# Optimization experiments

Measured on AMD Instinct MI355X. Metric: run time of the kernel, lower is better.

Reference implementation:

```python
import jax, jax.numpy as jnp
import numpy as np

N_CLASSES = 14
# n_classes==14 branch of the original: classes 0..6 -> 1 target maximum, 7..13 -> 2
NUM_TARGET = jnp.array([1] * 7 + [2] * 7, dtype=jnp.int32)
K_MAX = 2
MARGIN = 1.0  # margin=1, p=1 in the original loss_maxima calls


def _neighbor_max8(x):
    """Max over the 8-adjacent neighbors of each pixel (implicit 8-adjacency graph)."""
    H, W = x.shape
    pad = jnp.pad(x, 1, constant_values=-np.inf)
    shifts = [pad[di:di + H, dj:dj + W]
              for di in (0, 1, 2) for dj in (0, 1, 2) if not (di == 1 and dj == 1)]
    return jnp.max(jnp.stack(shifts, 0), axis=0)


def _channel_loss(x, k_target):
    """Surrogate of higra loss_maxima(graph, x, 'dynamics', 'volume', k, margin=1, p=1):
    strict 8-adjacency local maxima are ranked by importance (value above global min,
    a vectorizable proxy for dynamics/volume extinction); the top-k_target maxima pay a
    hinge max(0, margin - imp), all other maxima pay their importance (spurious peaks)."""
    imp = x - jnp.min(x)                      # persistence proxy, >= 0
    is_max = x > _neighbor_max8(x)            # strict local maxima on 8-adjacency
    total = jnp.sum(jnp.where(is_max, imp, 0.0))
    flat = jnp.where(is_max, imp, -np.inf).reshape(-1)
    topv, _ = jax.lax.top_k(flat, K_MAX)      # K_MAX=2 covers both branches
    valid = jnp.isfinite(topv) & (jnp.arange(K_MAX) < k_target)
    target_sum = jnp.sum(jnp.where(valid, topv, 0.0))
    spurious = total - target_sum             # penalize non-target maxima (volume proxy)
    hinge = jnp.sum(jnp.where(valid, jnp.maximum(MARGIN - topv, 0.0), 0.0))
    return spurious + hinge


def setup_inputs() -> dict:
    key = jax.random.key(0)
    k1, k2 = jax.random.split(key)
    inputs = jax.random.normal(k1, (1, N_CLASSES, 2048, 2048), dtype=jnp.float32)
    target = jax.random.randint(k2, (1, 2048, 2048), 0, N_CLASSES, dtype=jnp.int64)
    return {"inputs": inputs, "target": target}


def reference(inputs, target):
    # softmax=True path (logit inputs, as used in training)
    probs = jax.nn.softmax(inputs, axis=1)            # [1, C, H, W]
    onehot = jax.nn.one_hot(target, N_CLASSES, axis=1).astype(jnp.float32)
    assert probs.shape == onehot.shape                # mirrors original assert; onehot unused in loss
    chans = probs[0]                                  # only batch element 0, as in original
    losses = jax.vmap(_channel_loss)(chans, NUM_TARGET)
    return jnp.sum(losses) / N_CLASSES
```

## Files before the change

### kernel.cpp

```cpp
#include <hip/hip_runtime.h>

#define HH 2048
#define WW 2048
#define CC 14
#define TILE 30
#define NT 69
#define NB (NT*NT)
#define PB 4768

#define PINF __int_as_float(0x7f800000)
#define NINF __int_as_float(0xff800000)

template<int CTRL>
__device__ __forceinline__ float dppf(float x) {
  return __int_as_float(__builtin_amdgcn_update_dpp(0, __float_as_int(x), CTRL, 0xF, 0xF, true));
}
template<int CTRL>
__device__ __forceinline__ int dppi(int x) {
  return __builtin_amdgcn_update_dpp(0, x, CTRL, 0xF, 0xF, true);
}

struct Red { float mn, sm, t0, t1; int ct; };

template<int CTRL>
__device__ __forceinline__ void red_step(Red& r) {
  float omn = dppf<CTRL>(r.mn);
  float osm = dppf<CTRL>(r.sm);
  float o0  = dppf<CTRL>(r.t0);
  float o1  = dppf<CTRL>(r.t1);
  int   oc  = dppi<CTRL>(r.ct);
  r.mn = fminf(r.mn, omn);
  r.sm += osm;
  r.ct += oc;
  float n1 = fmaxf(fminf(r.t0, o0), fmaxf(r.t1, o1));
  r.t0 = fmaxf(r.t0, o0);
  r.t1 = n1;
}

__device__ __forceinline__ void wave_reduce(Red& r) {
  red_step<0xB1>(r);
  red_step<0x4E>(r);
  red_step<0x141>(r);
  red_step<0x140>(r);
  red_step<0x142>(r);
  red_step<0x143>(r);
}

__device__ __forceinline__ void merge2(float& a0, float& a1, float b0, float b1) {
  float n1 = fmaxf(fminf(a0, b0), fmaxf(a1, b1));
  a0 = fmaxf(a0, b0);
  a1 = n1;
}

__global__ __launch_bounds__(256, 2)
void k_main(const float* __restrict__ X, char* __restrict__ ws, int mode) {
  const int tid = threadIdx.x;
  const int bx = blockIdx.x, by = blockIdx.y;
  const int blk = by * NT + bx;
  const int rr = tid >> 3, c8 = tid & 7, c0 = c8 << 2;
  const int gr = by * TILE - 1 + rr;
  const int gc0 = bx * TILE - 1 + c0;
  const int lane = tid & 63, wv = tid >> 6;

  __shared__ float4 hplane[32][8];
  __shared__ float redmn[CC][4], redsm[CC][4], redt0[CC][4], redt1[CC][4];
  __shared__ int   redct[CC][4];

  float xv[CC][4];
  const bool rowok = ((unsigned)gr < (unsigned)HH);
  const int grc = rowok ? gr : 0;
  bool ok[4];
#pragma unroll
  for (int k = 0; k < 4; ++k) ok[k] = rowok && ((unsigned)(gc0 + k) < (unsigned)WW);
  const float* base = X + (size_t)grc * WW;
#pragma unroll
  for (int c = 0; c < CC; ++c) {
#pragma unroll
    for (int k = 0; k < 4; ++k) {
      int gck = gc0 + k;
      int gcc = ((unsigned)gck < (unsigned)WW) ? gck : 0;
      float v = base[(size_t)c * (size_t)(HH * WW) + gcc];
      xv[c][k] = ok[k] ? v : 0.0f;
    }
  }

#pragma unroll
  for (int k = 0; k < 4; ++k) {
    float m = xv[0][k];
#pragma unroll
    for (int c = 1; c < CC; ++c) m = fmaxf(m, xv[c][k]);
    float s = 0.f;
#pragma unroll
    for (int c = 0; c < CC; ++c) { float e = __expf(xv[c][k] - m); s += e; xv[c][k] = e; }
    float ri = 1.0f / s;
#pragma unroll
    for (int c = 0; c < CC; ++c) xv[c][k] = ok[k] ? xv[c][k] * ri : NINF;
  }

  bool inter[4];
  const bool rin = (rr >= 1) && (rr <= 30) && (gr < HH);
#pragma unroll
  for (int k = 0; k < 4; ++k) {
    int cc = c0 + k;
    inter[k] = rin && (cc >= 1) && (cc <= 30) && ((gc0 + k) < WW);
  }

  const int ru = (rr >= 1) ? rr - 1 : 0;
  const int rd = (rr <= 30) ? rr + 1 : 31;

#pragma unroll
  for (int c = 0; c < CC; ++c) {
    const float p0 = xv[c][0], p1 = xv[c][1], p2 = xv[c][2], p3 = xv[c][3];
    float pm1 = __shfl_up(p3, 1);   if (c8 == 0) pm1 = NINF;
    float pp4 = __shfl_down(p0, 1); if (c8 == 7) pp4 = NINF;
    const float hf0 = fmaxf(fmaxf(pm1, p0), p1);
    const float hf1 = fmaxf(fmaxf(p0, p1), p2);
    const float hf2 = fmaxf(fmaxf(p1, p2), p3);
    const float hf3 = fmaxf(fmaxf(p2, p3), pp4);
    const float hl0 = fmaxf(pm1, p1);
    const float hl1 = fmaxf(p0, p2);
    const float hl2 = fmaxf(p1, p3);
    const float hl3 = fmaxf(p2, pp4);
    __syncthreads();
    hplane[rr][c8] = make_float4(hf0, hf1, hf2, hf3);
    __syncthreads();
    const float4 up = hplane[ru][c8];
    const float4 dn = hplane[rd][c8];

    Red r; r.mn = PINF; r.sm = 0.f; r.ct = 0; r.t0 = NINF; r.t1 = NINF;
    {
      const float nb = fmaxf(fmaxf(up.x, dn.x), hl0);
      const bool im = inter[0] && (p0 > nb);
      r.mn = inter[0] ? fminf(r.mn, p0) : r.mn;
      if (im) { r.sm += p0; r.ct++; r.t1 = fmaxf(r.t1, fminf(r.t0, p0)); r.t0 = fmaxf(r.t0, p0); }
    }
    {
      const float nb = fmaxf(fmaxf(up.y, dn.y), hl1);
      const bool im = inter[1] && (p1 > nb);
      r.mn = inter[1] ? fminf(r.mn, p1) : r.mn;
      if (im) { r.sm += p1; r.ct++; r.t1 = fmaxf(r.t1, fminf(r.t0, p1)); r.t0 = fmaxf(r.t0, p1); }
    }
    {
      const float nb = fmaxf(fmaxf(up.z, dn.z), hl2);
      const bool im = inter[2] && (p2 > nb);
      r.mn = inter[2] ? fminf(r.mn, p2) : r.mn;
      if (im) { r.sm += p2; r.ct++; r.t1 = fmaxf(r.t1, fminf(r.t0, p2)); r.t0 = fmaxf(r.t0, p2); }
    }
    {
      const float nb = fmaxf(fmaxf(up.w, dn.w), hl3);
      const bool im = inter[3] && (p3 > nb);
      r.mn = inter[3] ? fminf(r.mn, p3) : r.mn;
      if (im) { r.sm += p3; r.ct++; r.t1 = fmaxf(r.t1, fminf(r.t0, p3)); r.t0 = fmaxf(r.t0, p3); }
    }

    wave_reduce(r);
    if (lane == 63) {
      redmn[c][wv] = r.mn; redsm[c][wv] = r.sm; redct[c][wv] = r.ct;
      redt0[c][wv] = r.t0; redt1[c][wv] = r.t1;
    }
  }

  __syncthreads();
  if (tid < CC) {
    const int c = tid;
    float mn = fminf(fminf(redmn[c][0], redmn[c][1]), fminf(redmn[c][2], redmn[c][3]));
    float sm = redsm[c][0] + redsm[c][1] + redsm[c][2] + redsm[c][3];
    int   ct = redct[c][0] + redct[c][1] + redct[c][2] + redct[c][3];
    float a0 = redt0[c][0], a1 = redt1[c][0];
    merge2(a0, a1, redt0[c][1], redt1[c][1]);
    merge2(a0, a1, redt0[c][2], redt1[c][2]);
    merge2(a0, a1, redt0[c][3], redt1[c][3]);

    if (mode == 0) {
      float* minb = (float*)(ws + 128);
      float* sumb = minb + CC * PB;
      int*   cntb = (int*)(sumb + CC * PB);
      float* t0b  = (float*)(cntb + CC * PB);
      float* t1b  = t0b + CC * PB;
      const int o = c * PB + blk;
      minb[o] = mn; sumb[o] = sm; cntb[o] = ct; t0b[o] = a0; t1b[o] = a1;
    } else {
      double*   wsum = (double*)ws;
      unsigned* wmin = (unsigned*)(ws + 128);
      int*      wcnt = (int*)(ws + 192);
      unsigned* s0   = (unsigned*)(ws + 256);
      unsigned* s1   = (unsigned*)(ws + 320);
      atomicMin(&wmin[c], __float_as_uint(mn));
      atomicAdd(&wsum[c], (double)sm);
      atomicAdd(&wcnt[c], ct);
      if (a0 != NINF) {
        unsigned b = __float_as_uint(a0);
        unsigned o = atomicMax(&s0[c], b);
        unsigned w2 = o < b ? o : b;
        if (w2) atomicMax(&s1[c], w2);
      }
      if (a1 != NINF) {
        unsigned b = __float_as_uint(a1);
        unsigned o = atomicMax(&s0[c], b);
        unsigned w2 = o < b ? o : b;
        if (w2) atomicMax(&s1[c], w2);
      }
    }
  }
}

__global__ void k_reduce(char* __restrict__ ws) {
  const int c = blockIdx.x, tid = threadIdx.x;
  double* lossb = (double*)ws;
  const float* minb = (const float*)(ws + 128);
  const float* sumb = minb + CC * PB;
  const int*   cntb = (const int*)(sumb + CC * PB);
  const float* t0b  = (const float*)(cntb + CC * PB);
  const float* t1b  = t0b + CC * PB;

  float mn = PINF; double sm = 0.0; int ct = 0; float t0 = NINF, t1 = NINF;
  const int o = c * PB;
  for (int i = tid; i < NB; i += 256) {
    mn = fminf(mn, minb[o + i]);
    sm += (double)sumb[o + i];
    ct += cntb[o + i];
    float b0 = t0b[o + i], b1 = t1b[o + i];
    t1 = fmaxf(t1, fminf(t0, b0)); t0 = fmaxf(t0, b0);
    t1 = fmaxf(t1, fminf(t0, b1)); t0 = fmaxf(t0, b1);
  }
  for (int m = 1; m < 64; m <<= 1) {
    float omn = __shfl_xor(mn, m);
    double osm = __shfl_xor(sm, m);
    int oc = __shfl_xor(ct, m);
    float o0 = __shfl_xor(t0, m), o1 = __shfl_xor(t1, m);
    mn = fminf(mn, omn); sm += osm; ct += oc;
    float n1 = fmaxf(fminf(t0, o0), fmaxf(t1, o1));
    t0 = fmaxf(t0, o0); t1 = n1;
  }
  __shared__ float smn[4], st0[4], st1[4];
  __shared__ double ssm[4];
  __shared__ int sct[4];
  const int lane = tid & 63, wv = tid >> 6;
  if (lane == 0) { smn[wv] = mn; ssm[wv] = sm; sct[wv] = ct; st0[wv] = t0; st1[wv] = t1; }
  __syncthreads();
  if (tid == 0) {
    mn = smn[0]; sm = ssm[0]; ct = sct[0]; t0 = st0[0]; t1 = st1[0];
    for (int w = 1; w < 4; ++w) {
      mn = fminf(mn, smn[w]); sm += ssm[w]; ct += sct[w];
      float n1 = fmaxf(fminf(t0, st0[w]), fmaxf(t1, st1[w]));
      t0 = fmaxf(t0, st0[w]); t1 = n1;
    }
    double minv = (double)mn;
    double total = sm - (double)ct * minv;
    const int kt = (c < 7) ? 1 : 2;
    double target = 0.0, hinge = 0.0;
    if (t0 != NINF) { double v = (double)t0 - minv; target += v; hinge += fmax(0.0, 1.0 - v); }
    if (kt == 2 && t1 != NINF) { double v = (double)t1 - minv; target += v; hinge += fmax(0.0, 1.0 - v); }
    lossb[c] = (total - target) + hinge;
  }
}

__global__ void k_final(const char* __restrict__ ws, float* __restrict__ out) {
  if (threadIdx.x == 0) {
    const double* lossb = (const double*)ws;
    double a = 0.0;
    for (int c = 0; c < CC; ++c) a += lossb[c];
    out[0] = (float)(a / (double)CC);
  }
}

__global__ void k_init_atomic(char* __restrict__ ws) {
  const int i = threadIdx.x;
  if (i < CC) {
    ((double*)ws)[i] = 0.0;
    ((unsigned*)(ws + 128))[i] = 0x7f800000u;
    ((int*)(ws + 192))[i] = 0;
    ((unsigned*)(ws + 256))[i] = 0u;
    ((unsigned*)(ws + 320))[i] = 0u;
  }
}

__global__ void k_final_atomic(const char* __restrict__ ws, float* __restrict__ out) {
  if (threadIdx.x == 0) {
    const double*   wsum = (const double*)ws;
    const unsigned* wmin = (const unsigned*)(ws + 128);
    const int*      wcnt = (const int*)(ws + 192);
    const unsigned* s0   = (const unsigned*)(ws + 256);
    const unsigned* s1   = (const unsigned*)(ws + 320);
    double a = 0.0;
    for (int c = 0; c < CC; ++c) {
      double minv = (double)__uint_as_float(wmin[c]);
      double total = wsum[c] - (double)wcnt[c] * minv;
      const int kt = (c < 7) ? 1 : 2;
      double target = 0.0, hinge = 0.0;
      if (s0[c]) { double v = (double)__uint_as_float(s0[c]) - minv; target += v; hinge += fmax(0.0, 1.0 - v); }
      if (kt == 2 && s1[c]) { double v = (double)__uint_as_float(s1[c]) - minv; target += v; hinge += fmax(0.0, 1.0 - v); }
      a += (total - target) + hinge;
    }
    out[0] = (float)(a / (double)CC);
  }
}

extern "C" void kernel_launch(void* const* d_in, const int* in_sizes, int n_in,
                              void* d_out, int out_size, void* d_ws, size_t ws_size,
                              hipStream_t stream) {
  const float* X = (const float*)d_in[0];
  float* out = (float*)d_out;
  char* ws = (char*)d_ws;
  const size_t needBuf = 128 + (size_t)5 * CC * PB * 4;
  dim3 grid(NT, NT);
  if (ws_size >= needBuf) {
    k_main<<<grid, 256, 0, stream>>>(X, ws, 0);
    k_reduce<<<CC, 256, 0, stream>>>(ws);
    k_final<<<1, 64, 0, stream>>>(ws, out);
  } else {
    k_init_atomic<<<1, 64, 0, stream>>>(ws);
    k_main<<<grid, 256, 0, stream>>>(X, ws, 1);
    k_final_atomic<<<1, 64, 0, stream>>>(ws, out);
  }
}
```

Baseline: 350.3 us.

## Batch channel halo exchange, vectorize interior loads, shorten wave reductions

```diff
diff --git a/kernel.cpp b/kernel.cpp
--- a/kernel.cpp
+++ b/kernel.cpp
@@ -2,6 +2,7 @@
 
 #define HH 2048
 #define WW 2048
+#define HW (HH*WW)
 #define CC 14
 #define TILE 30
 #define NT 69
@@ -10,6 +11,14 @@
 
 #define PINF __int_as_float(0x7f800000)
 #define NINF __int_as_float(0xff800000)
+
+typedef float f4 __attribute__((ext_vector_type(4)));
+
+__device__ __forceinline__ f4 load_f4u(const float* p) {
+  f4 v;
+  __builtin_memcpy(&v, p, 16);
+  return v;
+}
 
 template<int CTRL>
 __device__ __forceinline__ float dppf(float x) {
@@ -37,13 +46,11 @@
   r.t1 = n1;
 }
 
-__device__ __forceinline__ void wave_reduce(Red& r) {
+__device__ __forceinline__ void wave_reduce16(Red& r) {
   red_step<0xB1>(r);
   red_step<0x4E>(r);
   red_step<0x141>(r);
   red_step<0x140>(r);
-  red_step<0x142>(r);
-  red_step<0x143>(r);
 }
 
 __device__ __forceinline__ void merge2(float& a0, float& a1, float b0, float b1) {
@@ -52,7 +59,7 @@
   a1 = n1;
 }
 
-__global__ __launch_bounds__(256, 2)
+__global__ __launch_bounds__(256, 4)
 void k_main(const float* __restrict__ X, char* __restrict__ ws, int mode) {
   const int tid = threadIdx.x;
   const int bx = blockIdx.x, by = blockIdx.y;
@@ -62,25 +69,35 @@
   const int gc0 = bx * TILE - 1 + c0;
   const int lane = tid & 63, wv = tid >> 6;
 
-  __shared__ float4 hplane[32][8];
-  __shared__ float redmn[CC][4], redsm[CC][4], redt0[CC][4], redt1[CC][4];
-  __shared__ int   redct[CC][4];
+  __shared__ f4 hplane[7][32][8];
+  __shared__ float redmn[CC][16], redsm[CC][16], redt0[CC][16], redt1[CC][16];
+  __shared__ int   redct[CC][16];
 
   float xv[CC][4];
-  const bool rowok = ((unsigned)gr < (unsigned)HH);
-  const int grc = rowok ? gr : 0;
   bool ok[4];
-#pragma unroll
-  for (int k = 0; k < 4; ++k) ok[k] = rowok && ((unsigned)(gc0 + k) < (unsigned)WW);
-  const float* base = X + (size_t)grc * WW;
-#pragma unroll
-  for (int c = 0; c < CC; ++c) {
-#pragma unroll
-    for (int k = 0; k < 4; ++k) {
-      int gck = gc0 + k;
-      int gcc = ((unsigned)gck < (unsigned)WW) ? gck : 0;
-      float v = base[(size_t)c * (size_t)(HH * WW) + gcc];
-      xv[c][k] = ok[k] ? v : 0.0f;
+  const bool fast = (bx >= 1) && (bx <= 67) && (by >= 1) && (by <= 67);
+  if (fast) {
+    ok[0] = ok[1] = ok[2] = ok[3] = true;
+    const float* base = X + (size_t)gr * WW + gc0;
+#pragma unroll
+    for (int c = 0; c < CC; ++c) {
+      f4 v = load_f4u(base + (size_t)c * (size_t)HW);
+      xv[c][0] = v.x; xv[c][1] = v.y; xv[c][2] = v.z; xv[c][3] = v.w;
+    }
+  } else {
+    const bool rowok = ((unsigned)gr < (unsigned)HH);
+    const int grc = rowok ? gr : 0;
+#pragma unroll
+    for (int k = 0; k < 4; ++k) ok[k] = rowok && ((unsigned)(gc0 + k) < (unsigned)WW);
+    const float* base = X + (size_t)grc * WW;
+#pragma unroll
+    for (int c = 0; c < CC; ++c) {
+#pragma unroll
+      for (int k = 0; k < 4; ++k) {
+        int gck = gc0 + k;
+        int gcc = ((unsigned)gck < (unsigned)WW) ? gck : 0;
+        xv[c][k] = base[(size_t)c * (size_t)HW + gcc];
+      }
     }
   }
 
@@ -109,67 +126,82 @@
   const int rd = (rr <= 30) ? rr + 1 : 31;
 
 #pragma unroll
-  for (int c = 0; c < CC; ++c) {
-    const float p0 = xv[c][0], p1 = xv[c][1], p2 = xv[c][2], p3 = xv[c][3];
-    float pm1 = __shfl_up(p3, 1);   if (c8 == 0) pm1 = NINF;
-    float pp4 = __shfl_down(p0, 1); if (c8 == 7) pp4 = NINF;
-    const float hf0 = fmaxf(fmaxf(pm1, p0), p1);
-    const float hf1 = fmaxf(fmaxf(p0, p1), p2);
-    const float hf2 = fmaxf(fmaxf(p1, p2), p3);
-    const float hf3 = fmaxf(fmaxf(p2, p3), pp4);
-    const float hl0 = fmaxf(pm1, p1);
-    const float hl1 = fmaxf(p0, p2);
-    const float hl2 = fmaxf(p1, p3);
-    const float hl3 = fmaxf(p2, pp4);
+  for (int g = 0; g < 2; ++g) {
+    const int cbase = g * 7;
+#pragma unroll
+    for (int i = 0; i < 7; ++i) {
+      const int c = cbase + i;
+      const float p0 = xv[c][0], p1 = xv[c][1], p2 = xv[c][2], p3 = xv[c][3];
+      float pm1 = dppf<0x138>(p3); if (c8 == 0) pm1 = NINF;
+      float pp4 = dppf<0x130>(p0); if (c8 == 7) pp4 = NINF;
+      f4 hf;
+      hf.x = fmaxf(fmaxf(pm1, p0), p1);
+      hf.y = fmaxf(fmaxf(p0, p1), p2);
+      hf.z = fmaxf(fmaxf(p1, p2), p3);
+      hf.w = fmaxf(fmaxf(p2, p3), pp4);
+      hplane[i][rr][c8] = hf;
+    }
     __syncthreads();
-    hplane[rr][c8] = make_float4(hf0, hf1, hf2, hf3);
+#pragma unroll
+    for (int i = 0; i < 7; ++i) {
+      const int c = cbase + i;
+      const f4 up = hplane[i][ru][c8];
+      const f4 dn = hplane[i][rd][c8];
+      const float p0 = xv[c][0], p1 = xv[c][1], p2 = xv[c][2], p3 = xv[c][3];
+      float pm1 = dppf<0x138>(p3); if (c8 == 0) pm1 = NINF;
+      float pp4 = dppf<0x130>(p0); if (c8 == 7) pp4 = NINF;
+      const float hl0 = fmaxf(pm1, p1);
+      const float hl1 = fmaxf(p0, p2);
+      const float hl2 = fmaxf(p1, p3);
+      const float hl3 = fmaxf(p2, pp4);
+
+      Red r; r.mn = PINF; r.sm = 0.f; r.ct = 0; r.t0 = NINF; r.t1 = NINF;
+      {
+        const float nb = fmaxf(fmaxf(up.x, dn.x), hl0);
+        const bool im = inter[0] && (p0 > nb);
+        r.mn = inter[0] ? fminf(r.mn, p0) : r.mn;
+        if (im) { r.sm += p0; r.ct++; r.t1 = fmaxf(r.t1, fminf(r.t0, p0)); r.t0 = fmaxf(r.t0, p0); }
+      }
+      {
+        const float nb = fmaxf(fmaxf(up.y, dn.y), hl1);
+        const bool im = inter[1] && (p1 > nb);
+        r.mn = inter[1] ? fminf(r.mn, p1) : r.mn;
+        if (im) { r.sm += p1; r.ct++; r.t1 = fmaxf(r.t1, fminf(r.t0, p1)); r.t0 = fmaxf(r.t0, p1); }
+      }
+      {
+        const float nb = fmaxf(fmaxf(up.z, dn.z), hl2);
+        const bool im = inter[2] && (p2 > nb);
+        r.mn = inter[2] ? fminf(r.mn, p2) : r.mn;
+        if (im) { r.sm += p2; r.ct++; r.t1 = fmaxf(r.t1, fminf(r.t0, p2)); r.t0 = fmaxf(r.t0, p2); }
+      }
+      {
+        const float nb = fmaxf(fmaxf(up.w, dn.w), hl3);
+        const bool im = inter[3] && (p3 > nb);
+        r.mn = inter[3] ? fminf(r.mn, p3) : r.mn;
+        if (im) { r.sm += p3; r.ct++; r.t1 = fmaxf(r.t1, fminf(r.t0, p3)); r.t0 = fmaxf(r.t0, p3); }
+      }
+
+      wave_reduce16(r);
+      if ((lane & 15) == 0) {
+        const int s = (wv << 2) | (lane >> 4);
+        redmn[c][s] = r.mn; redsm[c][s] = r.sm; redct[c][s] = r.ct;
+        redt0[c][s] = r.t0; redt1[c][s] = r.t1;
+      }
+    }
     __syncthreads();
-    const float4 up = hplane[ru][c8];
-    const float4 dn = hplane[rd][c8];
-
-    Red r; r.mn = PINF; r.sm = 0.f; r.ct = 0; r.t0 = NINF; r.t1 = NINF;
-    {
-      const float nb = fmaxf(fmaxf(up.x, dn.x), hl0);
-      const bool im = inter[0] && (p0 > nb);
-      r.mn = inter[0] ? fminf(r.mn, p0) : r.mn;
-      if (im) { r.sm += p0; r.ct++; r.t1 = fmaxf(r.t1, fminf(r.t0, p0)); r.t0 = fmaxf(r.t0, p0); }
-    }
-    {
-      const float nb = fmaxf(fmaxf(up.y, dn.y), hl1);
-      const bool im = inter[1] && (p1 > nb);
-      r.mn = inter[1] ? fminf(r.mn, p1) : r.mn;
-      if (im) { r.sm += p1; r.ct++; r.t1 = fmaxf(r.t1, fminf(r.t0, p1)); r.t0 = fmaxf(r.t0, p1); }
-    }
-    {
-      const float nb = fmaxf(fmaxf(up.z, dn.z), hl2);
-      const bool im = inter[2] && (p2 > nb);
-      r.mn = inter[2] ? fminf(r.mn, p2) : r.mn;
-      if (im) { r.sm += p2; r.ct++; r.t1 = fmaxf(r.t1, fminf(r.t0, p2)); r.t0 = fmaxf(r.t0, p2); }
-    }
-    {
-      const float nb = fmaxf(fmaxf(up.w, dn.w), hl3);
-      const bool im = inter[3] && (p3 > nb);
-      r.mn = inter[3] ? fminf(r.mn, p3) : r.mn;
-      if (im) { r.sm += p3; r.ct++; r.t1 = fmaxf(r.t1, fminf(r.t0, p3)); r.t0 = fmaxf(r.t0, p3); }
-    }
-
-    wave_reduce(r);
-    if (lane == 63) {
-      redmn[c][wv] = r.mn; redsm[c][wv] = r.sm; redct[c][wv] = r.ct;
-      redt0[c][wv] = r.t0; redt1[c][wv] = r.t1;
-    }
-  }
-
-  __syncthreads();
+  }
+
   if (tid < CC) {
     const int c = tid;
-    float mn = fminf(fminf(redmn[c][0], redmn[c][1]), fminf(redmn[c][2], redmn[c][3]));
-    float sm = redsm[c][0] + redsm[c][1] + redsm[c][2] + redsm[c][3];
-    int   ct = redct[c][0] + redct[c][1] + redct[c][2] + redct[c][3];
-    float a0 = redt0[c][0], a1 = redt1[c][0];
-    merge2(a0, a1, redt0[c][1], redt1[c][1]);
-    merge2(a0, a1, redt0[c][2], redt1[c][2]);
-    merge2(a0, a1, redt0[c][3], redt1[c][3]);
+    float mn = PINF, sm = 0.f, a0 = NINF, a1 = NINF;
+    int ct = 0;
+#pragma unroll
+    for (int s = 0; s < 16; ++s) {
+      mn = fminf(mn, redmn[c][s]);
+      sm += redsm[c][s];
+      ct += redct[c][s];
+      merge2(a0, a1, redt0[c][s], redt1[c][s]);
+    }
 
     if (mode == 0) {
       float* minb = (float*)(ws + 128);
```

New measurement: 347.3 us. About the same (-0.9%).
